# Performance work log

Measured on AMD Instinct MI355X. Metric: run time of the kernel, lower is better.

The kernel has to match this reference:

```python
import jax, jax.numpy as jnp
import numpy as np

D_MODEL, N_HEADS, D_HEAD = 1024, 16, 64
BATCH, SEQ = 4, 2048


def setup_inputs() -> dict:
    key = jax.random.key(0)
    ks = jax.random.split(key, 10)
    s = 1.0 / np.sqrt(D_MODEL)
    x = jax.random.normal(ks[0], (BATCH, SEQ, D_MODEL), dtype=jnp.float32)
    attention_mask = jax.random.randint(ks[1], (BATCH, SEQ), 0, 2).astype(jnp.bool_)
    # guarantee at least one attended key per batch row (avoid all -inf softmax)
    attention_mask = attention_mask.at[:, 0].set(True)
    def lin(k):
        kw, kb = jax.random.split(k)
        W = jax.random.uniform(kw, (D_MODEL, D_MODEL), jnp.float32, -s, s)
        b = jax.random.uniform(kb, (D_MODEL,), jnp.float32, -s, s)
        return W, b
    Wq, bq = lin(ks[2]); Wk, bk = lin(ks[3]); Wv, bv = lin(ks[4]); Wo, bo = lin(ks[5])
    return {"x": x, "attention_mask": attention_mask,
            "Wq": Wq, "bq": bq, "Wk": Wk, "bk": bk,
            "Wv": Wv, "bv": bv, "Wo": Wo, "bo": bo}


def reference(x, attention_mask, Wq, bq, Wk, bk, Wv, bv, Wo, bo):
    B, S, _ = x.shape
    def proj(W, b):  # [B,S,d_model] -> [B,S,H,Dh]
        return (x @ W + b).reshape(B, S, N_HEADS, D_HEAD)
    q = proj(Wq, bq)
    k = proj(Wk, bk)
    v = proj(Wv, bv)
    scores = jnp.einsum('bqhd,bkhd->bhqk', q, k)  # [B,H,S,S]
    add_mask = jnp.where(attention_mask, 0.0, jnp.inf)[:, None, None, :]
    # faithful order: subtract mask, THEN scale (inf survives division)
    probs = jax.nn.softmax((scores - add_mask) / jnp.sqrt(jnp.float32(D_HEAD)), axis=-1)
    attn = jnp.einsum('bhqk,bkhd->bqhd', probs, v).reshape(B, S, N_HEADS * D_HEAD)
    return attn @ Wo + bo
```

## Files before the change

### kernel.cpp

```cpp
#include <hip/hip_runtime.h>
#include <hip/hip_bf16.h>
#include <math.h>

#define BATCH 4
#define SEQ   2048
#define DM    1024
#define NH    16
#define DH    64
#define MROWS (BATCH * SEQ)

typedef unsigned short ushort_t;
typedef unsigned int   uint_t;
typedef __attribute__((ext_vector_type(8))) short  short8;
typedef __attribute__((ext_vector_type(4))) float  float4v;

#define QSCALE 0.1803368801111244f

__device__ __forceinline__ ushort_t f2bf(float v) {
    uint_t u = __float_as_uint(v);
    u += 0x7FFFu + ((u >> 16) & 1u);
    return (ushort_t)(u >> 16);
}
__device__ __forceinline__ float bf2f(ushort_t h) {
    return __uint_as_float(((uint_t)h) << 16);
}
__device__ __forceinline__ void gload_lds16(const ushort_t* g, ushort_t* lds) {
    __builtin_amdgcn_global_load_lds(
        (const __attribute__((address_space(1))) void*)g,
        (__attribute__((address_space(3))) void*)lds, 16, 0, 0);
}

__global__ __launch_bounds__(256) void conv_x(
    const float* __restrict__ src, ushort_t* __restrict__ dst, int n4)
{
    int i = blockIdx.x * 256 + threadIdx.x;
    if (i >= n4) return;
    float4 v = ((const float4*)src)[i];
    ((ushort4*)dst)[i] = make_ushort4(f2bf(v.x), f2bf(v.y), f2bf(v.z), f2bf(v.w));
}

__global__ __launch_bounds__(256) void convT_w4(
    const float* __restrict__ W0, const float* __restrict__ W1,
    const float* __restrict__ W2, const float* __restrict__ W3,
    ushort_t* __restrict__ fused, ushort_t* __restrict__ woh,
    ushort_t* __restrict__ wol)
{
    __shared__ float sT[64][65];
    const int z = blockIdx.z;
    const float* W = (z == 0) ? W0 : (z == 1) ? W1 : (z == 2) ? W2 : W3;
    ushort_t* ht = (z < 3) ? fused + (size_t)z * 1024 * 1024 : woh;
    const int n0 = blockIdx.x * 64, k0 = blockIdx.y * 64;
    const int t = threadIdx.x;
#pragma unroll
    for (int i = 0; i < 16; i++) {
        int idx = t + i * 256, r = idx >> 6, c = idx & 63;
        sT[r][c] = W[(size_t)(k0 + r) * 1024 + n0 + c];
    }
    __syncthreads();
#pragma unroll
    for (int i = 0; i < 16; i++) {
        int idx = t + i * 256, r = idx >> 6, c = idx & 63;
        float v = sT[c][r];
        ushort_t h = f2bf(v);
        ht[(size_t)(n0 + r) * 1024 + k0 + c] = h;
        if (z == 3) wol[(size_t)(n0 + r) * 1024 + k0 + c] = f2bf(v - bf2f(h));
    }
}

#define BAR()   asm volatile("s_barrier" ::: "memory")
#define LGKM0() asm volatile("s_waitcnt lgkmcnt(0)" ::: "memory")
#define VMW6()  asm volatile("s_waitcnt vmcnt(6)" ::: "memory")

#define STAGE_A(BO, KT) do {                                                 \
    const ushort_t* _s = prowA + (size_t)((KT) & 15) * 64;                   \
    gload_lds16(_s,         &smem[(BO) + dstw]);                             \
    gload_lds16(_s + 65536, &smem[(BO) + 4096 + dstw]);                      \
  } while (0)

#define STAGE_B(BO, KT) do {                                                 \
    const ushort_t* _s = prowB + (size_t)((KT) & 15) * 64;                   \
    gload_lds16(_s,          &smem[(BO) + 8192  + dstw]);                    \
    gload_lds16(_s + 65536,  &smem[(BO) + 12288 + dstw]);                    \
    gload_lds16(_s + 131072, &smem[(BO) + 16384 + dstw]);                    \
    gload_lds16(_s + 196608, &smem[(BO) + 20480 + dstw]);                    \
  } while (0)

#define LOAD_AV(BO) do {                                                     \
    _Pragma("unroll")                                                        \
    for (int mf = 0; mf < 4; mf++) {                                         \
      av[mf][0] = *(const short8*)&smem[(BO) + aAm + mf * 1024 + aA0];       \
      av[mf][1] = *(const short8*)&smem[(BO) + aAm + mf * 1024 + aA1];       \
    }                                                                        \
  } while (0)

#define LOAD_BV(BO, NQ) do {                                                 \
    _Pragma("unroll")                                                        \
    for (int nf = 0; nf < 2; nf++) {                                         \
      bvf[nf][0] = *(const short8*)&smem[(BO) + 8192 + aBn + (NQ) * 2048 +   \
                                         nf * 1024 + aA0];                   \
      bvf[nf][1] = *(const short8*)&smem[(BO) + 8192 + aBn + (NQ) * 2048 +   \
                                         nf * 1024 + aA1];                   \
    }                                                                        \
  } while (0)

#define MFMA_H(NQ) do {                                                      \
    __builtin_amdgcn_s_setprio(1);                                           \
    _Pragma("unroll")                                                        \
    for (int kk = 0; kk < 2; kk++)                                           \
      _Pragma("unroll")                                                      \
      for (int nf = 0; nf < 2; nf++)                                         \
        _Pragma("unroll")                                                    \
        for (int mf = 0; mf < 4; mf++)                                       \
          acc[mf][(NQ) * 2 + nf] =                                           \
              __builtin_amdgcn_mfma_f32_16x16x32_bf16(                       \
                  av[mf][kk], bvf[nf][kk], acc[mf][(NQ) * 2 + nf], 0, 0, 0); \
    __builtin_amdgcn_s_setprio(0);                                           \
  } while (0)

__global__ __launch_bounds__(512, 2) void gemm_qkv(
    const ushort_t* __restrict__ A, const ushort_t* __restrict__ Bt,
    const float* __restrict__ bq, const float* __restrict__ bk,
    const float* __restrict__ bv, const int* __restrict__ mask,
    ushort_t* __restrict__ Qh, ushort_t* __restrict__ Kh,
    ushort_t* __restrict__ Vt)
{
    __shared__ __align__(16) ushort_t smem[73728];
    const int t = threadIdx.x, lane = t & 63, w = t >> 6;

    int bid = blockIdx.y * 12 + blockIdx.x;
    bid = (bid & 7) * 96 + (bid >> 3);
    const int n0 = (bid % 12) * 256, m0 = (bid / 12) * 128;

    const int wm = w >> 2, wn = w & 3;
    const int lq = lane >> 4, lc = lane & 15;
    const int gl = (lane & 7) ^ ((lane >> 3) & 7);
    const int sect = n0 >> 10;
    const float* bsel = (sect == 0) ? bq : (sect == 1) ? bk : bv;
    const float scl = (sect == 0) ? QSCALE : 1.0f;

    const ushort_t* prowA = A  + (size_t)(m0 + w * 8 + (lane >> 3)) * 1024 + gl * 8;
    const ushort_t* prowB = Bt + (size_t)(n0 + w * 8 + (lane >> 3)) * 1024 + gl * 8;
    const int dstw = w * 512;

    const int aA0 = lc * 64 + ((lq ^ (lc & 7)) * 8);
    const int aA1 = lc * 64 + (((4 + lq) ^ (lc & 7)) * 8);
    const int aAm = wm * 4096;
    const int aBn = wn * 4096;

    float4v acc[4][4];
#pragma unroll
    for (int i = 0; i < 4; i++)
#pragma unroll
        for (int j = 0; j < 4; j++) acc[i][j] = (float4v)(0.0f);

    short8 av[4][2], bvf[2][2];

    STAGE_A(0, 0); STAGE_B(0, 0); STAGE_A(24576, 1); STAGE_B(24576, 1);
    VMW6();
    BAR();

    int bc = 0, bs = 49152;
    for (int kt = 0; kt < 16; kt++) {
        LOAD_AV(bc); LOAD_BV(bc, 0); STAGE_A(bs, kt + 2);
        BAR(); LGKM0(); MFMA_H(0); BAR();
        LOAD_BV(bc, 1); STAGE_B(bs, kt + 2);
        BAR(); LGKM0(); MFMA_H(1); VMW6(); BAR();
        bc = (bc == 49152) ? 0 : bc + 24576;
        bs = (bs == 49152) ? 0 : bs + 24576;
    }

#pragma unroll
    for (int nf = 0; nf < 4; nf++) {
        const int nn = (n0 + wn * 64 + nf * 16 + lc) & 1023;
        const float bvv = bsel[nn];
        const int h = nn >> 6, d = nn & 63;
#pragma unroll
        for (int mf = 0; mf < 4; mf++) {
            const int mbase = m0 + wm * 64 + mf * 16 + lq * 4;
            const int b = mbase >> 11, s0 = mbase & 2047;
            int mk[4] = {1, 1, 1, 1};
            if (sect != 0) {
                const int4 m4 = *(const int4*)&mask[b * 2048 + s0];
                mk[0] = m4.x; mk[1] = m4.y; mk[2] = m4.z; mk[3] = m4.w;
            }
            if (sect == 2) {
                ushort_t hh[4];
#pragma unroll
                for (int r = 0; r < 4; r++)
                    hh[r] = mk[r] ? f2bf(acc[mf][nf][r] + bvv) : (ushort_t)0;
                *(ushort4*)&Vt[((size_t)(b * 16 + h) * 64 + d) * 2048 + s0] =
                    make_ushort4(hh[0], hh[1], hh[2], hh[3]);
            } else {
                ushort_t* dst = (sect == 0) ? Qh : Kh;
#pragma unroll
                for (int r = 0; r < 4; r++)
                    dst[((size_t)(b * 16 + h) * 2048 + s0 + r) * 64 + d] =
                        mk[r] ? f2bf((acc[mf][nf][r] + bvv) * scl) : (ushort_t)0;
            }
        }
    }
}

#undef STAGE_A
#undef STAGE_B
#undef LOAD_AV
#undef LOAD_BV
#undef MFMA_H
#undef BAR
#undef LGKM0
#undef VMW6

__global__ __launch_bounds__(256) void gemm_split3(
    const ushort_t* __restrict__ Ah, const ushort_t* __restrict__ Al,
    const ushort_t* __restrict__ Bh, const ushort_t* __restrict__ Bl,
    const float* __restrict__ bias, float* __restrict__ out)
{
    __shared__ __align__(16) ushort_t smem[16384];
    const int t = threadIdx.x, lane = t & 63, w = t >> 6;
    const int n0 = blockIdx.x * 128, m0 = blockIdx.y * 128;
    const int wm = (w >> 1) * 64, wn = (w & 1) * 64;
    const int lq = lane >> 4, lc = lane & 15;
    const int gl = (lane & 3) ^ ((lane >> 3) & 3);
    const int irow = lane >> 2;

    float4v acc[4][4];
#pragma unroll
    for (int i = 0; i < 4; i++)
#pragma unroll
        for (int j = 0; j < 4; j++) acc[i][j] = (float4v)(0.0f);

    const ushort_t* plane = (w == 0) ? Ah : (w == 1) ? Al : (w == 2) ? Bh : Bl;
    const size_t prow = (size_t)(((w < 2) ? m0 : n0) + irow) * 1024 + gl * 8;

    for (int k0 = 0; k0 < 1024; k0 += 32) {
        __syncthreads();
#pragma unroll
        for (int j = 0; j < 8; j++)
            gload_lds16(plane + prow + (size_t)j * 16384 + k0, &smem[w * 4096 + j * 512]);
        __syncthreads();

        short8 ah[4], al[4];
#pragma unroll
        for (int mt = 0; mt < 4; mt++) {
            const int r = wm + mt * 16 + lc;
            const int off = r * 32 + ((lq ^ ((r >> 1) & 3)) * 8);
            ah[mt] = *(const short8*)&smem[off];
            al[mt] = *(const short8*)&smem[4096 + off];
        }
#pragma unroll
        for (int nt = 0; nt < 4; nt++) {
            const int r = wn + nt * 16 + lc;
            const int off = r * 32 + ((lq ^ ((r >> 1) & 3)) * 8);
            short8 bh = *(const short8*)&smem[8192 + off];
            short8 bl = *(const short8*)&smem[12288 + off];
#pragma unroll
            for (int mt = 0; mt < 4; mt++) {
                acc[mt][nt] = __builtin_amdgcn_mfma_f32_16x16x32_bf16(ah[mt], bh, acc[mt][nt], 0, 0, 0);
                acc[mt][nt] = __builtin_amdgcn_mfma_f32_16x16x32_bf16(al[mt], bh, acc[mt][nt], 0, 0, 0);
                acc[mt][nt] = __builtin_amdgcn_mfma_f32_16x16x32_bf16(ah[mt], bl, acc[mt][nt], 0, 0, 0);
            }
        }
    }

#pragma unroll
    for (int nt = 0; nt < 4; nt++) {
        const int n = n0 + wn + nt * 16 + lc;
        const float bvv = bias[n];
#pragma unroll
        for (int mt = 0; mt < 4; mt++)
#pragma unroll
            for (int r = 0; r < 4; r++) {
                const int m = m0 + wm + mt * 16 + lq * 4 + r;
                out[(size_t)m * 1024 + n] = acc[mt][nt][r] + bvv;
            }
    }
}

__global__ __launch_bounds__(256, 4) void flash_mfma(
    const ushort_t* __restrict__ Q, const ushort_t* __restrict__ K,
    const ushort_t* __restrict__ Vt, const int* __restrict__ mask,
    ushort_t* __restrict__ Oh, ushort_t* __restrict__ Ol)
{
    __shared__ __align__(16) ushort_t smem[16384];
    const int t = threadIdx.x, lane = t & 63, w = t >> 6;
    const int q0 = blockIdx.x * 128;
    const int bh = blockIdx.y, b = bh >> 4, h = bh & 15;
    const int lq = lane >> 4, lc = lane & 15;
    const int wm = w * 32;
    const int gl = (lane & 7) ^ ((lane >> 3) & 7);
    const int lc7 = lc & 7;

    const short8 onesf = (short8)(lc == 0 ? (short)0x3F80 : (short)0);

    int cnt;
    {
        const int4* mrow = (const int4*)(mask + b * SEQ);
        const int4 a = mrow[t * 2], c = mrow[t * 2 + 1];
        cnt = (a.x == 0) + (a.y == 0) + (a.z == 0) + (a.w == 0) +
              (c.x == 0) + (c.y == 0) + (c.z == 0) + (c.w == 0);
#pragma unroll
        for (int off = 1; off < 64; off <<= 1) cnt += __shfl_xor(cnt, off);
        if (lane == 0) ((float*)&smem[8192])[w] = (float)cnt;
    }
#pragma unroll
    for (int j = 0; j < 4; j++) {
        const int i = w * 4 + j;
        gload_lds16(Q + ((size_t)bh * SEQ + q0 + i * 8 + (lane >> 3)) * 64 + gl * 8,
                    &smem[i * 512]);
    }
    __syncthreads();
    const float nmaskf = ((const float*)&smem[8192])[0] + ((const float*)&smem[8192])[1] +
                         ((const float*)&smem[8192])[2] + ((const float*)&smem[8192])[3];

    short8 aq[2][2];
#pragma unroll
    for (int mt = 0; mt < 2; mt++)
#pragma unroll
        for (int kk = 0; kk < 2; kk++) {
            const int r = wm + mt * 16 + lc;
            aq[mt][kk] = *(const short8*)&smem[r * 64 + (((kk * 4 + lq) ^ (r & 7)) * 8)];
        }

    int aK[2], aPw[4], aPr[2];
#pragma unroll
    for (int kk = 0; kk < 2; kk++) {
        aK[kk]  = lc * 64 + (((kk * 4 + lq) ^ lc7) * 8);
        aPr[kk] = wm * 64 + aK[kk];
    }
#pragma unroll
    for (int kt4 = 0; kt4 < 4; kt4++)
        aPw[kt4] = wm * 64 + lc * 64 + (((kt4 * 2 + (lq >> 1)) ^ lc7) * 8) + (lq & 1) * 4;

    const ushort_t* gsrc;
    int gstride;
    int dstbase;
    int jstride;
    if (w < 2) {
        gsrc = K + ((size_t)bh * SEQ + w * 32 + (lane >> 3)) * 64 + gl * 8;
        gstride = 64 * 64;  dstbase = 8192 + w * 2048;  jstride = 512;
    } else {
        gsrc = Vt + ((size_t)bh * 64 + (w - 2) * 32 + (lane >> 3)) * SEQ + gl * 8;
        gstride = 64;       dstbase = 12288 + (w - 2) * 2048;  jstride = 8 * 2048;
    }

    float4v O[2][4];
    float4v lacc[2];
#pragma unroll
    for (int mt = 0; mt < 2; mt++) {
#pragma unroll
        for (int nt = 0; nt < 4; nt++) O[mt][nt] = (float4v)(0.0f);
        lacc[mt] = (float4v)(0.0f);
    }

    for (int kt = 0; kt < 32; kt++) {
        __syncthreads();
#pragma unroll
        for (int j = 0; j < 4; j++)
            gload_lds16(gsrc + j * jstride, &smem[dstbase + j * 512]);
        gsrc += gstride;
        __syncthreads();

        float4v sc[4][2];
#pragma unroll
        for (int kt4 = 0; kt4 < 4; kt4++)
#pragma unroll
            for (int mt = 0; mt < 2; mt++) sc[kt4][mt] = (float4v)(0.0f);
#pragma unroll
        for (int kk = 0; kk < 2; kk++) {
#pragma unroll
            for (int kt4 = 0; kt4 < 4; kt4++) {
                short8 ak = *(const short8*)&smem[8192 + kt4 * 1024 + aK[kk]];
#pragma unroll
                for (int mt = 0; mt < 2; mt++)
                    sc[kt4][mt] = __builtin_amdgcn_mfma_f32_16x16x32_bf16(ak, aq[mt][kk], sc[kt4][mt], 0, 0, 0);
            }
        }

#pragma unroll
        for (int kt4 = 0; kt4 < 4; kt4++) {
#pragma unroll
            for (int mt = 0; mt < 2; mt++) {
                const float p0 = __builtin_amdgcn_exp2f(sc[kt4][mt][0]);
                const float p1 = __builtin_amdgcn_exp2f(sc[kt4][mt][1]);
                const float p2 = __builtin_amdgcn_exp2f(sc[kt4][mt][2]);
                const float p3 = __builtin_amdgcn_exp2f(sc[kt4][mt][3]);
                __hip_bfloat162 pk01 = __float22bfloat162_rn(make_float2(p0, p1));
                __hip_bfloat162 pk23 = __float22bfloat162_rn(make_float2(p2, p3));
                *(uint2*)&smem[mt * 1024 + aPw[kt4]] =
                    make_uint2(*(const uint_t*)&pk01, *(const uint_t*)&pk23);
            }
        }

#pragma unroll
        for (int kk = 0; kk < 2; kk++) {
            short8 ap[2];
#pragma unroll
            for (int mt = 0; mt < 2; mt++)
                ap[mt] = *(const short8*)&smem[mt * 1024 + aPr[kk]];
#pragma unroll
            for (int mt = 0; mt < 2; mt++)
                lacc[mt] = __builtin_amdgcn_mfma_f32_16x16x32_bf16(ap[mt], onesf, lacc[mt], 0, 0, 0);
#pragma unroll
            for (int nt = 0; nt < 4; nt++) {
                short8 bv = *(const short8*)&smem[12288 + nt * 1024 + aK[kk]];
#pragma unroll
                for (int mt = 0; mt < 2; mt++)
                    O[mt][nt] = __builtin_amdgcn_mfma_f32_16x16x32_bf16(ap[mt], bv, O[mt][nt], 0, 0, 0);
            }
        }
    }

#pragma unroll
    for (int mt = 0; mt < 2; mt++) {
#pragma unroll
        for (int r = 0; r < 4; r++) {
            const float lsum = __shfl(lacc[mt][r], lane & 48) - nmaskf;
            const float inv = 1.0f / lsum;
            const int srow = q0 + wm + mt * 16 + lq * 4 + r;
#pragma unroll
            for (int nt = 0; nt < 4; nt++) {
                const float v = O[mt][nt][r] * inv;
                const ushort_t hh = f2bf(v);
                const size_t idx = ((size_t)(b * SEQ + srow)) * 1024 + h * 64 + nt * 16 + lc;
                Oh[idx] = hh;
                Ol[idx] = f2bf(v - bf2f(hh));
            }
        }
    }
}

extern "C" void kernel_launch(void* const* d_in, const int* in_sizes, int n_in,
                              void* d_out, int out_size, void* d_ws, size_t ws_size,
                              hipStream_t stream) {
    const float* x    = (const float*)d_in[0];
    const int*   mask = (const int*)d_in[1];
    const float* Wq   = (const float*)d_in[2];
    const float* bq   = (const float*)d_in[3];
    const float* Wk   = (const float*)d_in[4];
    const float* bk   = (const float*)d_in[5];
    const float* Wv   = (const float*)d_in[6];
    const float* bv   = (const float*)d_in[7];
    const float* Wo   = (const float*)d_in[8];
    const float* bo   = (const float*)d_in[9];
    float* out = (float*)d_out;

    ushort_t* p = (ushort_t*)d_ws;
    const size_t PLANE  = (size_t)MROWS * DM;
    const size_t WPLANE = (size_t)DM * DM;
    ushort_t* xh  = p;  p += PLANE;
    ushort_t* wf  = p;  p += 3 * WPLANE;
    ushort_t* woh = p;  p += WPLANE;
    ushort_t* wol = p;  p += WPLANE;
    ushort_t* Qh  = p;  p += PLANE;
    ushort_t* Kh  = p;  p += PLANE;
    ushort_t* Vth = p;  p += PLANE;
    ushort_t* Ath = p;  p += PLANE;
    ushort_t* Atl = p;  p += PLANE;

    dim3 blk(256);
    hipLaunchKernelGGL(conv_x, dim3(8192), blk, 0, stream, x, xh, 2097152);
    hipLaunchKernelGGL(convT_w4, dim3(16, 16, 4), blk, 0, stream,
                       Wq, Wk, Wv, Wo, wf, woh, wol);
    hipLaunchKernelGGL(gemm_qkv, dim3(12, 64), dim3(512), 0, stream,
                       xh, wf, bq, bk, bv, mask, Qh, Kh, Vth);
    hipLaunchKernelGGL(flash_mfma, dim3(16, 64), blk, 0, stream,
                       Qh, Kh, Vth, mask, Ath, Atl);
    hipLaunchKernelGGL(gemm_split3, dim3(8, 64), blk, 0, stream,
                       Ath, Atl, woh, wol, bo, out);
}
```

Before: 333.3 us.

## Double-buffer K/V tiles and widen flash attention blocks to 512 threads

```diff
diff --git a/kernel.cpp b/kernel.cpp
--- a/kernel.cpp
+++ b/kernel.cpp
@@ -206,9 +206,6 @@
 #undef LOAD_AV
 #undef LOAD_BV
 #undef MFMA_H
-#undef BAR
-#undef LGKM0
-#undef VMW6
 
 __global__ __launch_bounds__(256) void gemm_split3(
     const ushort_t* __restrict__ Ah, const ushort_t* __restrict__ Al,
@@ -276,14 +273,14 @@
     }
 }
 
-__global__ __launch_bounds__(256, 4) void flash_mfma(
+__global__ __launch_bounds__(512, 4) void flash_mfma(
     const ushort_t* __restrict__ Q, const ushort_t* __restrict__ K,
     const ushort_t* __restrict__ Vt, const int* __restrict__ mask,
     ushort_t* __restrict__ Oh, ushort_t* __restrict__ Ol)
 {
-    __shared__ __align__(16) ushort_t smem[16384];
+    __shared__ __align__(16) ushort_t smem[32768];
     const int t = threadIdx.x, lane = t & 63, w = t >> 6;
-    const int q0 = blockIdx.x * 128;
+    const int q0 = blockIdx.x * 256;
     const int bh = blockIdx.y, b = bh >> 4, h = bh & 15;
     const int lq = lane >> 4, lc = lane & 15;
     const int wm = w * 32;
@@ -292,15 +289,12 @@
 
     const short8 onesf = (short8)(lc == 0 ? (short)0x3F80 : (short)0);
 
-    int cnt;
     {
-        const int4* mrow = (const int4*)(mask + b * SEQ);
-        const int4 a = mrow[t * 2], c = mrow[t * 2 + 1];
-        cnt = (a.x == 0) + (a.y == 0) + (a.z == 0) + (a.w == 0) +
-              (c.x == 0) + (c.y == 0) + (c.z == 0) + (c.w == 0);
+        const int4 a = ((const int4*)(mask + b * SEQ))[t];
+        int cnt = (a.x == 0) + (a.y == 0) + (a.z == 0) + (a.w == 0);
 #pragma unroll
         for (int off = 1; off < 64; off <<= 1) cnt += __shfl_xor(cnt, off);
-        if (lane == 0) ((float*)&smem[8192])[w] = (float)cnt;
+        if (lane == 0) ((float*)&smem[28672])[w] = (float)cnt;
     }
 #pragma unroll
     for (int j = 0; j < 4; j++) {
@@ -308,9 +302,24 @@
         gload_lds16(Q + ((size_t)bh * SEQ + q0 + i * 8 + (lane >> 3)) * 64 + gl * 8,
                     &smem[i * 512]);
     }
+    const ushort_t* gsrc;
+    int gstride, jstride, dstb;
+    if (w < 4) {
+        gsrc = K + ((size_t)bh * SEQ + w * 16 + (lane >> 3)) * 64 + gl * 8;
+        gstride = 64 * 64;  jstride = 8 * 64;   dstb = 16384 + w * 1024;
+    } else {
+        gsrc = Vt + ((size_t)bh * 64 + (w - 4) * 16 + (lane >> 3)) * SEQ + gl * 8;
+        gstride = 64;       jstride = 8 * SEQ;  dstb = 24576 + (w - 4) * 1024;
+    }
+    gload_lds16(gsrc,           &smem[dstb]);
+    gload_lds16(gsrc + jstride, &smem[dstb + 512]);
+    gsrc += gstride;
+
     __syncthreads();
-    const float nmaskf = ((const float*)&smem[8192])[0] + ((const float*)&smem[8192])[1] +
-                         ((const float*)&smem[8192])[2] + ((const float*)&smem[8192])[3];
+
+    const float* cs = (const float*)&smem[28672];
+    const float nmaskf = cs[0] + cs[1] + cs[2] + cs[3] +
+                         cs[4] + cs[5] + cs[6] + cs[7];
 
     short8 aq[2][2];
 #pragma unroll
@@ -331,18 +340,6 @@
     for (int kt4 = 0; kt4 < 4; kt4++)
         aPw[kt4] = wm * 64 + lc * 64 + (((kt4 * 2 + (lq >> 1)) ^ lc7) * 8) + (lq & 1) * 4;
 
-    const ushort_t* gsrc;
-    int gstride;
-    int dstbase;
-    int jstride;
-    if (w < 2) {
-        gsrc = K + ((size_t)bh * SEQ + w * 32 + (lane >> 3)) * 64 + gl * 8;
-        gstride = 64 * 64;  dstbase = 8192 + w * 2048;  jstride = 512;
-    } else {
-        gsrc = Vt + ((size_t)bh * 64 + (w - 2) * 32 + (lane >> 3)) * SEQ + gl * 8;
-        gstride = 64;       dstbase = 12288 + (w - 2) * 2048;  jstride = 8 * 2048;
-    }
-
     float4v O[2][4];
     float4v lacc[2];
 #pragma unroll
@@ -352,41 +349,45 @@
         lacc[mt] = (float4v)(0.0f);
     }
 
+    __syncthreads();
+
     for (int kt = 0; kt < 32; kt++) {
-        __syncthreads();
-#pragma unroll
-        for (int j = 0; j < 4; j++)
-            gload_lds16(gsrc + j * jstride, &smem[dstbase + j * 512]);
-        gsrc += gstride;
-        __syncthreads();
-
-        float4v sc[4][2];
-#pragma unroll
-        for (int kt4 = 0; kt4 < 4; kt4++)
-#pragma unroll
-            for (int mt = 0; mt < 2; mt++) sc[kt4][mt] = (float4v)(0.0f);
-#pragma unroll
-        for (int kk = 0; kk < 2; kk++) {
-#pragma unroll
-            for (int kt4 = 0; kt4 < 4; kt4++) {
-                short8 ak = *(const short8*)&smem[8192 + kt4 * 1024 + aK[kk]];
-#pragma unroll
-                for (int mt = 0; mt < 2; mt++)
-                    sc[kt4][mt] = __builtin_amdgcn_mfma_f32_16x16x32_bf16(ak, aq[mt][kk], sc[kt4][mt], 0, 0, 0);
-            }
+        const int cur = (kt & 1) * 4096;
+        const int nxt = cur ^ 4096;
+
+        if (kt < 31) {
+            gload_lds16(gsrc,           &smem[dstb + nxt]);
+            gload_lds16(gsrc + jstride, &smem[dstb + nxt + 512]);
+            gsrc += gstride;
         }
 
 #pragma unroll
         for (int kt4 = 0; kt4 < 4; kt4++) {
-#pragma unroll
-            for (int mt = 0; mt < 2; mt++) {
-                const float p0 = __builtin_amdgcn_exp2f(sc[kt4][mt][0]);
-                const float p1 = __builtin_amdgcn_exp2f(sc[kt4][mt][1]);
-                const float p2 = __builtin_amdgcn_exp2f(sc[kt4][mt][2]);
-                const float p3 = __builtin_amdgcn_exp2f(sc[kt4][mt][3]);
+            float4v s0 = (float4v)(0.0f), s1 = (float4v)(0.0f);
+#pragma unroll
+            for (int kk = 0; kk < 2; kk++) {
+                short8 ak = *(const short8*)&smem[16384 + cur + kt4 * 1024 + aK[kk]];
+                s0 = __builtin_amdgcn_mfma_f32_16x16x32_bf16(ak, aq[0][kk], s0, 0, 0, 0);
+                s1 = __builtin_amdgcn_mfma_f32_16x16x32_bf16(ak, aq[1][kk], s1, 0, 0, 0);
+            }
+            {
+                const float p0 = __builtin_amdgcn_exp2f(s0[0]);
+                const float p1 = __builtin_amdgcn_exp2f(s0[1]);
+                const float p2 = __builtin_amdgcn_exp2f(s0[2]);
+                const float p3 = __builtin_amdgcn_exp2f(s0[3]);
                 __hip_bfloat162 pk01 = __float22bfloat162_rn(make_float2(p0, p1));
                 __hip_bfloat162 pk23 = __float22bfloat162_rn(make_float2(p2, p3));
-                *(uint2*)&smem[mt * 1024 + aPw[kt4]] =
+                *(uint2*)&smem[aPw[kt4]] =
+                    make_uint2(*(const uint_t*)&pk01, *(const uint_t*)&pk23);
+            }
+            {
+                const float p0 = __builtin_amdgcn_exp2f(s1[0]);
+                const float p1 = __builtin_amdgcn_exp2f(s1[1]);
+                const float p2 = __builtin_amdgcn_exp2f(s1[2]);
+                const float p3 = __builtin_amdgcn_exp2f(s1[3]);
+                __hip_bfloat162 pk01 = __float22bfloat162_rn(make_float2(p0, p1));
+                __hip_bfloat162 pk23 = __float22bfloat162_rn(make_float2(p2, p3));
+                *(uint2*)&smem[1024 + aPw[kt4]] =
                     make_uint2(*(const uint_t*)&pk01, *(const uint_t*)&pk23);
             }
         }
@@ -397,17 +398,22 @@
 #pragma unroll
             for (int mt = 0; mt < 2; mt++)
                 ap[mt] = *(const short8*)&smem[mt * 1024 + aPr[kk]];
+            __builtin_amdgcn_s_setprio(1);
 #pragma unroll
             for (int mt = 0; mt < 2; mt++)
                 lacc[mt] = __builtin_amdgcn_mfma_f32_16x16x32_bf16(ap[mt], onesf, lacc[mt], 0, 0, 0);
 #pragma unroll
             for (int nt = 0; nt < 4; nt++) {
-                short8 bv = *(const short8*)&smem[12288 + nt * 1024 + aK[kk]];
+                short8 bv = *(const short8*)&smem[24576 + cur + nt * 1024 + aK[kk]];
 #pragma unroll
                 for (int mt = 0; mt < 2; mt++)
                     O[mt][nt] = __builtin_amdgcn_mfma_f32_16x16x32_bf16(ap[mt], bv, O[mt][nt], 0, 0, 0);
             }
-        }
+            __builtin_amdgcn_s_setprio(0);
+        }
+
+        asm volatile("s_waitcnt vmcnt(0)" ::: "memory");
+        asm volatile("s_barrier" ::: "memory");
     }
 
 #pragma unroll
@@ -428,6 +434,10 @@
         }
     }
 }
+
+#undef BAR
+#undef LGKM0
+#undef VMW6
 
 extern "C" void kernel_launch(void* const* d_in, const int* in_sizes, int n_in,
                               void* d_out, int out_size, void* d_ws, size_t ws_size,
@@ -463,7 +473,7 @@
                        Wq, Wk, Wv, Wo, wf, woh, wol);
     hipLaunchKernelGGL(gemm_qkv, dim3(12, 64), dim3(512), 0, stream,
                        xh, wf, bq, bk, bv, mask, Qh, Kh, Vth);
-    hipLaunchKernelGGL(flash_mfma, dim3(16, 64), blk, 0, stream,
+    hipLaunchKernelGGL(flash_mfma, dim3(8, 64), dim3(512), 0, stream,
                        Qh, Kh, Vth, mask, Ath, Atl);
     hipLaunchKernelGGL(gemm_split3, dim3(8, 64), blk, 0, stream,
                        Ath, Atl, woh, wol, bo, out);
```

Result: faster. 311.8 us (-6.4%).
